# Optimization experiments

Measured on AMD Instinct MI355X. Metric: run time of the kernel, lower is better.

## Reference

```python
import jax, jax.numpy as jnp
import numpy as np

S = 8192        # total packed tokens
HID = 3072      # hidden_size
NHQ = 24        # query heads
NHKV = 8        # kv heads (GQA)
HD = 128        # head dim
NM = 2          # modalities (experts); tokens assumed modality-sorted: first half mod0, second half mod1
CHUNK = 1024    # ranged attention: 8 equal q/k ranges (block-diagonal)
NB = S // CHUNK
EPS = 1e-6


def setup_inputs() -> dict:
    key = jax.random.key(0)
    ks = jax.random.split(key, 4)
    s = 0.02
    qkv_out = (NHQ + 2 * NHKV) * HD
    # rotary tables: cos/sin of shape (S, HD/2)
    pos = jnp.arange(S, dtype=jnp.float32)
    inv_freq = 1.0 / (10000.0 ** (jnp.arange(0, HD, 2, dtype=jnp.float32) / HD))
    freqs = pos[:, None] * inv_freq[None, :]
    return {
        "x": jax.random.normal(ks[0], (S, HID), jnp.float32),
        "w_qkv": jax.random.normal(ks[1], (NM, qkv_out, HID), jnp.float32) * s,
        "b_qkv": jnp.zeros((NM, qkv_out), jnp.float32),
        "q_norm_w": jnp.zeros((NM, HD), jnp.float32),
        "k_norm_w": jnp.zeros((NM, HD), jnp.float32),
        "cos": jnp.cos(freqs),
        "sin": jnp.sin(freqs),
        "w_out": jax.random.normal(ks[2], (NM, HID, NHQ * HD), jnp.float32) * s,
        "b_out": jnp.zeros((NM, HID), jnp.float32),
    }


def _rms(t):
    # MultiModalityRMSNorm.rms: fp32 rsqrt(mean(x^2)+eps)
    return t * jax.lax.rsqrt(jnp.mean(t * t, axis=-1, keepdims=True) + EPS)


def _rotate_half(t):
    x1, x2 = jnp.split(t, 2, axis=-1)
    return jnp.concatenate([-x2, x1], axis=-1)


def reference(x, w_qkv, b_qkv, q_norm_w, k_norm_w, cos, sin, w_out, b_out):
    half = S // NM
    xm = x.reshape(NM, half, HID)                        # modality-dispatched tokens
    # per-modality (MoE) qkv projection: [m, t, out]
    qkv = jnp.einsum('mti,moi->mto', xm, w_qkv) + b_qkv[:, None, :]
    q, k, v = jnp.split(qkv, [NHQ * HD, (NHQ + NHKV) * HD], axis=-1)
    q = q.reshape(NM, half, NHQ, HD)
    k = k.reshape(NM, half, NHKV, HD)
    v = v.reshape(NM, half, NHKV, HD)
    # per-modality QK RMSNorm over head_dim, weight init zeros -> scale (w+1)
    q = _rms(q) * (q_norm_w[:, None, None, :] + 1.0)
    k = _rms(k) * (k_norm_w[:, None, None, :] + 1.0)
    # RoPE (non-interleaved): cos/sin (S, HD/2) -> (m, t, 1, HD) via (2 d) repeat
    cosm = cos.reshape(NM, half, HD // 2)
    sinm = sin.reshape(NM, half, HD // 2)
    cos2 = jnp.concatenate([cosm, cosm], axis=-1)[:, :, None, :]
    sin2 = jnp.concatenate([sinm, sinm], axis=-1)[:, :, None, :]
    q = q * cos2 + _rotate_half(q) * sin2
    k = k * cos2 + _rotate_half(k) * sin2
    # undispatch back to packed token order (modality-sorted identity permutation)
    qs = q.reshape(S, NHQ, HD)
    ks = k.reshape(S, NHKV, HD)
    vs = v.reshape(S, NHKV, HD)
    # ranged (block-diagonal) flash attention: NB equal q/k ranges of CHUNK tokens
    qb = qs.reshape(NB, CHUNK, NHQ, HD)
    kb = jnp.repeat(ks.reshape(NB, CHUNK, NHKV, HD), NHQ // NHKV, axis=2)  # GQA expand
    vb = jnp.repeat(vs.reshape(NB, CHUNK, NHKV, HD), NHQ // NHKV, axis=2)
    scale = HD ** -0.5
    scores = jnp.einsum('bqhd,bkhd->bhqk', qb, kb) * scale
    attn = jax.nn.softmax(scores, axis=-1)
    ob = jnp.einsum('bhqk,bkhd->bqhd', attn, vb)
    o = ob.reshape(NM, half, NHQ * HD)
    # per-modality output projection
    out = jnp.einsum('mti,moi->mto', o, w_out) + b_out[:, None, :]
    return out.reshape(S, HID)
```

## Files before the change

kernel.cpp:

```cpp
#include <hip/hip_runtime.h>
#include <hip/hip_bf16.h>


typedef __bf16 bf16;
typedef __attribute__((ext_vector_type(8))) __bf16 bf16x8;
typedef __attribute__((ext_vector_type(4))) __bf16 bf16x4;
typedef __attribute__((ext_vector_type(4))) float f32x4;

#define S_TOT 8192
#define HID 3072
#define NHQ 24
#define NHKV 8
#define HD 128
#define QKV_OUT 5120
#define CHUNKT 1024

__device__ inline void gload_lds16(const void* g, void* l) {
  __builtin_amdgcn_global_load_lds((const __attribute__((address_space(1))) void*)g,
                                   (__attribute__((address_space(3))) void*)l, 16, 0, 0);
}

__device__ inline f32x4 mfma16(bf16x8 a, bf16x8 b, f32x4 c) {
  return __builtin_amdgcn_mfma_f32_16x16x32_bf16(a, b, c, 0, 0, 0);
}

__global__ __launch_bounds__(256) void cvt_kernel(const float* __restrict__ in,
                                                  bf16* __restrict__ out, int n4) {
  int idx = blockIdx.x * 256 + threadIdx.x;
  int stride = gridDim.x * 256;
  for (int i = idx; i < n4; i += stride) {
    float4 v = reinterpret_cast<const float4*>(in)[i];
    bf16x4 o = {(bf16)v.x, (bf16)v.y, (bf16)v.z, (bf16)v.w};
    reinterpret_cast<bf16x4*>(out)[i] = o;
  }
}

template <int OUT_BF16>
__global__ __launch_bounds__(512, 2) void gemm256(const bf16* __restrict__ A,
                                                  const bf16* __restrict__ B,
                                                  const float* __restrict__ bias,
                                                  void* __restrict__ Cv,
                                                  int M, int N, int K) {
  __shared__ bf16 lds[65536];
  const int tid = threadIdx.x;
  const int l = tid & 63;
  const int w = tid >> 6;
  const int wr = w >> 2, wc = w & 3;
  const int lm = l & 15, lg = l >> 4;

  const int nwg = gridDim.x;
  const int id = blockIdx.x;
  const int swzid = (id & 7) * (nwg >> 3) + (id >> 3);
  const int xt = N >> 8, yt = M >> 8;
  const int bn = swzid % xt;
  const int rem = swzid / xt;
  const int bm = rem % yt;
  const int mz = rem / yt;

  const bf16* Ag = A + (size_t)mz * M * K + (size_t)(bm * 256) * K;
  const bf16* Bg = B + (size_t)mz * N * K + (size_t)(bn * 256) * K;
  const float* biasg = bias + (size_t)mz * N;

  const int srow = tid >> 3;
  const int scolb = ((tid & 7) * 16) ^ ((srow & 7) << 4);
  const bf16* Asrc = Ag + (size_t)srow * K + (scolb >> 1);
  const bf16* Bsrc = Bg + (size_t)srow * K + (scolb >> 1);
  bf16* ldsA = lds;
  bf16* ldsB = lds + 32768;

  auto stA = [&](int buf, int q, int t) {
    gload_lds16(Asrc + (size_t)(q * 64) * K + t * 64,
                ldsA + buf * 16384 + q * 4096 + tid * 8);
  };
  auto stB = [&](int buf, int q, int t) {
    gload_lds16(Bsrc + (size_t)(q * 64) * K + t * 64,
                ldsB + buf * 16384 + q * 4096 + tid * 8);
  };

  const int xmb = (lm & 7) << 4;
  const int cb0 = (lg * 16) ^ xmb;
  const int cb1 = cb0 ^ 64;
  const int aoff0 = (wr * 128 + lm) * 64 + (cb0 >> 1);
  const int aoff1 = (wr * 128 + lm) * 64 + (cb1 >> 1);
  const int boff0 = (wc * 64 + lm) * 64 + (cb0 >> 1);
  const int boff1 = (wc * 64 + lm) * 64 + (cb1 >> 1);

  const int NT = K >> 6;
  f32x4 acc[8][4] = {};

#pragma unroll
  for (int q = 0; q < 4; ++q) stA(0, q, 0);
#pragma unroll
  for (int q = 0; q < 4; ++q) stB(0, q, 0);
#pragma unroll
  for (int q = 0; q < 4; ++q) stA(1, q, 1);
  stB(1, 0, 1);
  stB(1, 1, 1);
  asm volatile("s_waitcnt vmcnt(6)" ::: "memory");
  __builtin_amdgcn_s_barrier();

  for (int T = 0; T < NT; ++T) {
    const int cbuf = T & 1, nbuf = cbuf ^ 1;
    const bf16* Ac = ldsA + cbuf * 16384;
    const bf16* Bc = ldsB + cbuf * 16384;
    const bool s1 = (T + 1) < NT;
    const bool s2 = (T + 2) < NT;
    bf16x8 alo[4][2], ahi[4][2], blo[2][2], bhi[2][2];

#pragma unroll
    for (int i = 0; i < 4; ++i) {
      alo[i][0] = *(const bf16x8*)(Ac + aoff0 + i * 1024);
      alo[i][1] = *(const bf16x8*)(Ac + aoff1 + i * 1024);
    }
#pragma unroll
    for (int j = 0; j < 2; ++j) {
      blo[j][0] = *(const bf16x8*)(Bc + boff0 + j * 1024);
      blo[j][1] = *(const bf16x8*)(Bc + boff1 + j * 1024);
    }
    if (s1) { stB(nbuf, 2, T + 1); stB(nbuf, 3, T + 1); }
    __builtin_amdgcn_s_barrier();
    asm volatile("s_waitcnt lgkmcnt(0)" ::: "memory");
    __builtin_amdgcn_s_setprio(1);
#pragma unroll
    for (int i = 0; i < 4; ++i)
#pragma unroll
      for (int j = 0; j < 2; ++j) {
        acc[i][j] = mfma16(alo[i][0], blo[j][0], acc[i][j]);
        acc[i][j] = mfma16(alo[i][1], blo[j][1], acc[i][j]);
      }
    __builtin_amdgcn_s_setprio(0);
    __builtin_amdgcn_s_barrier();

#pragma unroll
    for (int j = 0; j < 2; ++j) {
      bhi[j][0] = *(const bf16x8*)(Bc + boff0 + (j + 2) * 1024);
      bhi[j][1] = *(const bf16x8*)(Bc + boff1 + (j + 2) * 1024);
    }
    if (s2) { stA(cbuf, 0, T + 2); stA(cbuf, 2, T + 2); }
    __builtin_amdgcn_s_barrier();
    asm volatile("s_waitcnt lgkmcnt(0)" ::: "memory");
    __builtin_amdgcn_s_setprio(1);
#pragma unroll
    for (int i = 0; i < 4; ++i)
#pragma unroll
      for (int j = 0; j < 2; ++j) {
        acc[i][j + 2] = mfma16(alo[i][0], bhi[j][0], acc[i][j + 2]);
        acc[i][j + 2] = mfma16(alo[i][1], bhi[j][1], acc[i][j + 2]);
      }
    __builtin_amdgcn_s_setprio(0);
    __builtin_amdgcn_s_barrier();

#pragma unroll
    for (int i = 0; i < 4; ++i) {
      ahi[i][0] = *(const bf16x8*)(Ac + aoff0 + (i + 4) * 1024);
      ahi[i][1] = *(const bf16x8*)(Ac + aoff1 + (i + 4) * 1024);
    }
    if (s2) { stB(cbuf, 0, T + 2); stB(cbuf, 1, T + 2); }
    __builtin_amdgcn_s_barrier();
    asm volatile("s_waitcnt lgkmcnt(0)" ::: "memory");
    __builtin_amdgcn_s_setprio(1);
#pragma unroll
    for (int i = 0; i < 4; ++i)
#pragma unroll
      for (int j = 0; j < 2; ++j) {
        acc[i + 4][j] = mfma16(ahi[i][0], blo[j][0], acc[i + 4][j]);
        acc[i + 4][j] = mfma16(ahi[i][1], blo[j][1], acc[i + 4][j]);
      }
    __builtin_amdgcn_s_setprio(0);
    __builtin_amdgcn_s_barrier();

    if (s2) { stA(cbuf, 1, T + 2); stA(cbuf, 3, T + 2); }
    __builtin_amdgcn_s_barrier();
    __builtin_amdgcn_s_setprio(1);
#pragma unroll
    for (int i = 0; i < 4; ++i)
#pragma unroll
      for (int j = 0; j < 2; ++j) {
        acc[i + 4][j + 2] = mfma16(ahi[i][0], bhi[j][0], acc[i + 4][j + 2]);
        acc[i + 4][j + 2] = mfma16(ahi[i][1], bhi[j][1], acc[i + 4][j + 2]);
      }
    __builtin_amdgcn_s_setprio(0);
    if (s2)
      asm volatile("s_waitcnt vmcnt(6)" ::: "memory");
    else
      asm volatile("s_waitcnt vmcnt(0)" ::: "memory");
    __builtin_amdgcn_s_barrier();
  }

  const int row0 = bm * 256 + wr * 128 + lg * 4;
  const int col0 = bn * 256 + wc * 64 + lm;
#pragma unroll
  for (int j = 0; j < 4; ++j) {
    const int col = col0 + j * 16;
    const float bv = biasg[col];
#pragma unroll
    for (int i = 0; i < 8; ++i)
#pragma unroll
      for (int r = 0; r < 4; ++r) {
        const int row = row0 + i * 16 + r;
        const float v = acc[i][j][r] + bv;
        if (OUT_BF16)
          ((bf16*)Cv)[(size_t)mz * M * N + (size_t)row * N + col] = (bf16)v;
        else
          ((float*)Cv)[(size_t)mz * M * N + (size_t)row * N + col] = v;
      }
  }
}

__global__ __launch_bounds__(256) void rmsrope_kernel(bf16* __restrict__ qkv,
                                                      const float* __restrict__ qw,
                                                      const float* __restrict__ kw,
                                                      const float* __restrict__ cosT,
                                                      const float* __restrict__ sinT) {
  int gid = blockIdx.x * 4 + (threadIdx.x >> 6);
  int l = threadIdx.x & 63;
  int tok = gid >> 5;
  int slot = gid & 31;
  int mz = tok >> 12;
  bf16* p;
  const float* wv;
  if (slot < NHQ) {
    p = qkv + (size_t)tok * QKV_OUT + slot * HD;
    wv = qw + mz * HD;
  } else {
    p = qkv + (size_t)tok * QKV_OUT + HID + (slot - NHQ) * HD;
    wv = kw + mz * HD;
  }
  int d = l * 2;
  float x0 = (float)p[d];
  float x1 = (float)p[d + 1];
  float ss = x0 * x0 + x1 * x1;
#pragma unroll
  for (int m = 1; m < 64; m <<= 1) ss += __shfl_xor(ss, m);
  float rn = rsqrtf(ss * (1.0f / 128.0f) + 1e-6f);
  float n0 = x0 * rn * (wv[d] + 1.0f);
  float n1 = x1 * rn * (wv[d + 1] + 1.0f);
  float o0 = __shfl_xor(n0, 32);
  float o1 = __shfl_xor(n1, 32);
  int ci = d & 63;
  float2 cv = *reinterpret_cast<const float2*>(cosT + (size_t)tok * 64 + ci);
  float2 sv = *reinterpret_cast<const float2*>(sinT + (size_t)tok * 64 + ci);
  float sgn = (l < 32) ? -1.0f : 1.0f;
  p[d] = (bf16)(n0 * cv.x + sgn * o0 * sv.x);
  p[d + 1] = (bf16)(n1 * cv.y + sgn * o1 * sv.y);
}

__global__ __launch_bounds__(256) void attn_kernel(const bf16* __restrict__ qkv,
                                                   bf16* __restrict__ o) {
  constexpr float CEXP = 0.12753139626334912f;
  const int tid = threadIdx.x;
  const int l = tid & 63;
  const int w = tid >> 6;
  const int sq = blockIdx.x;
  const int h = blockIdx.y;
  const int blk = blockIdx.z;
  const int kvh = h / 3;
  const int qtok0 = blk * CHUNKT + sq * 128 + w * 32;
  const int ktok0 = blk * CHUNKT;

  __shared__ bf16 KP[128 * 136];
  __shared__ bf16 Vt[128 * 136];

  bf16x8 qf[2][4];
#pragma unroll
  for (int i = 0; i < 2; ++i) {
    const bf16* qp =
        qkv + (size_t)(qtok0 + i * 16 + (l & 15)) * QKV_OUT + h * HD + (l >> 4) * 8;
#pragma unroll
    for (int c = 0; c < 4; ++c) qf[i][c] = *reinterpret_cast<const bf16x8*>(qp + c * 32);
  }

  f32x4 of[2][8] = {};
  float mrow[2][4], lrow[2][4];
#pragma unroll
  for (int i = 0; i < 2; ++i)
#pragma unroll
    for (int r = 0; r < 4; ++r) {
      mrow[i][r] = -1e30f;
      lrow[i][r] = 0.0f;
    }

  for (int c = 0; c < 8; ++c) {
    __syncthreads();
    const int kt = ktok0 + c * 128;
#pragma unroll
    for (int it = 0; it < 8; ++it) {
      int task = it * 256 + tid;
      int key = task >> 4, dc = task & 15;
      *reinterpret_cast<bf16x8*>(&KP[key * 136 + dc * 8]) =
          *reinterpret_cast<const bf16x8*>(
              qkv + (size_t)(kt + key) * QKV_OUT + HID + kvh * HD + dc * 8);
    }
#pragma unroll
    for (int it = 0; it < 8; ++it) {
      int task = it * 256 + tid;
      int key = task & 127, dc = task >> 7;
      bf16x8 vv = *reinterpret_cast<const bf16x8*>(
          qkv + (size_t)(kt + key) * QKV_OUT + HID + NHKV * HD + kvh * HD + dc * 8);
#pragma unroll
      for (int jj = 0; jj < 8; ++jj) Vt[(dc * 8 + jj) * 136 + key] = vv[jj];
    }
    __syncthreads();

    f32x4 sacc[2][8] = {};
#pragma unroll
    for (int kd = 0; kd < 4; ++kd) {
      bf16x8 kb[8];
#pragma unroll
      for (int j = 0; j < 8; ++j)
        kb[j] = *reinterpret_cast<const bf16x8*>(
            &KP[(j * 16 + (l & 15)) * 136 + kd * 32 + (l >> 4) * 8]);
#pragma unroll
      for (int i = 0; i < 2; ++i)
#pragma unroll
        for (int j = 0; j < 8; ++j) sacc[i][j] = mfma16(qf[i][kd], kb[j], sacc[i][j]);
    }

    float alpha[2][4];
#pragma unroll
    for (int i = 0; i < 2; ++i) {
#pragma unroll
      for (int r = 0; r < 4; ++r) {
        float mx = sacc[i][0][r];
#pragma unroll
        for (int j = 1; j < 8; ++j) mx = fmaxf(mx, sacc[i][j][r]);
        mx = fmaxf(mx, __shfl_xor(mx, 1));
        mx = fmaxf(mx, __shfl_xor(mx, 2));
        mx = fmaxf(mx, __shfl_xor(mx, 4));
        mx = fmaxf(mx, __shfl_xor(mx, 8));
        float mnew = fmaxf(mrow[i][r], mx);
        float al = exp2f((mrow[i][r] - mnew) * CEXP);
        mrow[i][r] = mnew;
        float ps = 0.0f;
#pragma unroll
        for (int j = 0; j < 8; ++j) {
          float pv = exp2f((sacc[i][j][r] - mnew) * CEXP);
          sacc[i][j][r] = pv;
          ps += pv;
        }
        ps += __shfl_xor(ps, 1);
        ps += __shfl_xor(ps, 2);
        ps += __shfl_xor(ps, 4);
        ps += __shfl_xor(ps, 8);
        lrow[i][r] = lrow[i][r] * al + ps;
        alpha[i][r] = al;
      }
    }
#pragma unroll
    for (int i = 0; i < 2; ++i)
#pragma unroll
      for (int j = 0; j < 8; ++j)
#pragma unroll
        for (int r = 0; r < 4; ++r) of[i][j][r] *= alpha[i][r];

    __syncthreads();
    bf16* P = KP + w * (32 * 136);
#pragma unroll
    for (int i = 0; i < 2; ++i)
#pragma unroll
      for (int j = 0; j < 8; ++j)
#pragma unroll
        for (int r = 0; r < 4; ++r)
          P[(i * 16 + (l >> 4) * 4 + r) * 136 + j * 16 + (l & 15)] = (bf16)sacc[i][j][r];

#pragma unroll
    for (int kk = 0; kk < 4; ++kk) {
      bf16x8 pa[2];
#pragma unroll
      for (int i = 0; i < 2; ++i)
        pa[i] = *reinterpret_cast<const bf16x8*>(
            &P[(i * 16 + (l & 15)) * 136 + kk * 32 + (l >> 4) * 8]);
#pragma unroll
      for (int j = 0; j < 8; ++j) {
        bf16x8 bv = *reinterpret_cast<const bf16x8*>(
            &Vt[(j * 16 + (l & 15)) * 136 + kk * 32 + (l >> 4) * 8]);
        of[0][j] = mfma16(pa[0], bv, of[0][j]);
        of[1][j] = mfma16(pa[1], bv, of[1][j]);
      }
    }
  }

#pragma unroll
  for (int i = 0; i < 2; ++i) {
#pragma unroll
    for (int r = 0; r < 4; ++r) {
      float inv = 1.0f / lrow[i][r];
      int row = qtok0 + i * 16 + (l >> 4) * 4 + r;
      bf16* orow = o + (size_t)row * HID + h * HD + (l & 15);
#pragma unroll
      for (int j = 0; j < 8; ++j) orow[j * 16] = (bf16)(of[i][j][r] * inv);
    }
  }
}

extern "C" void kernel_launch(void* const* d_in, const int* in_sizes, int n_in,
                              void* d_out, int out_size, void* d_ws, size_t ws_size,
                              hipStream_t stream) {
  const float* x = (const float*)d_in[0];
  const float* wqkv = (const float*)d_in[1];
  const float* bqkv = (const float*)d_in[2];
  const float* qnw = (const float*)d_in[3];
  const float* knw = (const float*)d_in[4];
  const float* cosT = (const float*)d_in[5];
  const float* sinT = (const float*)d_in[6];
  const float* wout = (const float*)d_in[7];
  const float* bout = (const float*)d_in[8];
  float* out = (float*)d_out;

  char* ws = (char*)d_ws;
  bf16* xb = (bf16*)ws;
  ws += (size_t)S_TOT * HID * 2;
  bf16* wqkvb = (bf16*)ws;
  ws += (size_t)2 * QKV_OUT * HID * 2;
  bf16* qkv = (bf16*)ws;
  bf16* ob = xb;
  bf16* woutb = wqkvb;

  cvt_kernel<<<2048, 256, 0, stream>>>(x, xb, S_TOT * HID / 4);
  cvt_kernel<<<2048, 256, 0, stream>>>(wqkv, wqkvb, 2 * QKV_OUT * HID / 4);

  gemm256<1><<<(QKV_OUT / 256) * (4096 / 256) * 2, 512, 0, stream>>>(
      xb, wqkvb, bqkv, qkv, 4096, QKV_OUT, HID);

  cvt_kernel<<<2048, 256, 0, stream>>>(wout, woutb, 2 * HID * HID / 4);

  rmsrope_kernel<<<(S_TOT * (NHQ + NHKV)) / 4, 256, 0, stream>>>(qkv, qnw, knw, cosT, sinT);

  attn_kernel<<<dim3(8, NHQ, 8), 256, 0, stream>>>(qkv, ob);

  gemm256<0><<<(HID / 256) * (4096 / 256) * 2, 512, 0, stream>>>(
      ob, woutb, bout, out, 4096, HID, HID);
}
```

Measured before the change: 1.136 ms.

## Double-buffer K/V tiles with register prefetch and XOR-swizzled LDS in attention

The attention kernel now processes 64-key tiles instead of 128, keeps two LDS buffers for K and V, and prefetches the next tile into registers during compute. It writes that tile to the alternate buffer after the PV step, so there is one barrier per iteration instead of three. Padded LDS rows are replaced by XOR swizzles on K, transposed V and a dedicated per-wave P buffer, and s_setprio wraps the MFMA bursts. The goal is to hide global-load latency and cut LDS bank conflicts and syncs. The cost is more registers for the prefetch, which could reduce occupancy.

After: 1.237 ms. +9.0%, slower.

```diff
diff --git a/kernel.cpp b/kernel.cpp
--- a/kernel.cpp
+++ b/kernel.cpp
@@ -248,27 +248,64 @@
 __global__ __launch_bounds__(256) void attn_kernel(const bf16* __restrict__ qkv,
                                                    bf16* __restrict__ o) {
   constexpr float CEXP = 0.12753139626334912f;
+  constexpr int NCH = CHUNKT / 64;
   const int tid = threadIdx.x;
   const int l = tid & 63;
   const int w = tid >> 6;
+  const int lm = l & 15, lg = l >> 4;
   const int sq = blockIdx.x;
   const int h = blockIdx.y;
   const int blk = blockIdx.z;
   const int kvh = h / 3;
   const int qtok0 = blk * CHUNKT + sq * 128 + w * 32;
-  const int ktok0 = blk * CHUNKT;
-
-  __shared__ bf16 KP[128 * 136];
-  __shared__ bf16 Vt[128 * 136];
+
+  __shared__ bf16 Ks[2][64 * 128];
+  __shared__ bf16 Vs[2][128 * 64];
+  __shared__ bf16 Ps[4][32 * 64];
 
   bf16x8 qf[2][4];
 #pragma unroll
   for (int i = 0; i < 2; ++i) {
-    const bf16* qp =
-        qkv + (size_t)(qtok0 + i * 16 + (l & 15)) * QKV_OUT + h * HD + (l >> 4) * 8;
+    const bf16* qp = qkv + (size_t)(qtok0 + i * 16 + lm) * QKV_OUT + h * HD + lg * 8;
 #pragma unroll
     for (int c = 0; c < 4; ++c) qf[i][c] = *reinterpret_cast<const bf16x8*>(qp + c * 32);
   }
+
+  const bf16* Kg = qkv + (size_t)(blk * CHUNKT) * QKV_OUT + HID + kvh * HD;
+  const bf16* Vg = Kg + NHKV * HD;
+  const int krow = tid >> 4;
+  const int kdc8 = (tid & 15) * 8;
+  const int vkey = tid & 63;
+  const int vdc0 = tid >> 6;
+
+  bf16x8 kreg[4], vreg[4];
+  auto loadKV = [&](int c) {
+    const bf16* kp = Kg + (size_t)(c * 64) * QKV_OUT;
+    const bf16* vp = Vg + (size_t)(c * 64) * QKV_OUT;
+#pragma unroll
+    for (int it = 0; it < 4; ++it)
+      kreg[it] = *reinterpret_cast<const bf16x8*>(
+          kp + (size_t)(it * 16 + krow) * QKV_OUT + kdc8);
+#pragma unroll
+    for (int it = 0; it < 4; ++it)
+      vreg[it] = *reinterpret_cast<const bf16x8*>(
+          vp + (size_t)vkey * QKV_OUT + (it * 4 + vdc0) * 8);
+  };
+  auto writeKV = [&](int buf) {
+#pragma unroll
+    for (int it = 0; it < 4; ++it) {
+      int key = it * 16 + krow;
+      *reinterpret_cast<bf16x8*>(&Ks[buf][key * 128 + (kdc8 ^ ((key & 7) << 3))]) =
+          kreg[it];
+    }
+#pragma unroll
+    for (int it = 0; it < 4; ++it) {
+      int d0 = (it * 4 + vdc0) * 8;
+#pragma unroll
+      for (int jj = 0; jj < 8; ++jj)
+        Vs[buf][(d0 + jj) * 64 + (vkey ^ (jj << 3))] = vreg[it][jj];
+    }
+  };
 
   f32x4 of[2][8] = {};
   float mrow[2][4], lrow[2][4];
@@ -280,40 +317,32 @@
       lrow[i][r] = 0.0f;
     }
 
-  for (int c = 0; c < 8; ++c) {
-    __syncthreads();
-    const int kt = ktok0 + c * 128;
-#pragma unroll
-    for (int it = 0; it < 8; ++it) {
-      int task = it * 256 + tid;
-      int key = task >> 4, dc = task & 15;
-      *reinterpret_cast<bf16x8*>(&KP[key * 136 + dc * 8]) =
-          *reinterpret_cast<const bf16x8*>(
-              qkv + (size_t)(kt + key) * QKV_OUT + HID + kvh * HD + dc * 8);
-    }
-#pragma unroll
-    for (int it = 0; it < 8; ++it) {
-      int task = it * 256 + tid;
-      int key = task & 127, dc = task >> 7;
-      bf16x8 vv = *reinterpret_cast<const bf16x8*>(
-          qkv + (size_t)(kt + key) * QKV_OUT + HID + NHKV * HD + kvh * HD + dc * 8);
-#pragma unroll
-      for (int jj = 0; jj < 8; ++jj) Vt[(dc * 8 + jj) * 136 + key] = vv[jj];
-    }
-    __syncthreads();
-
-    f32x4 sacc[2][8] = {};
+  loadKV(0);
+  writeKV(0);
+  __syncthreads();
+
+  const int swz = (lm & 7) << 3;
+  for (int c = 0; c < NCH; ++c) {
+    const int cur = c & 1;
+    if (c + 1 < NCH) loadKV(c + 1);
+    const bf16* Kc = Ks[cur];
+    const bf16* Vc = Vs[cur];
+    bf16* Pw = Ps[w];
+
+    f32x4 sacc[2][4] = {};
 #pragma unroll
     for (int kd = 0; kd < 4; ++kd) {
-      bf16x8 kb[8];
-#pragma unroll
-      for (int j = 0; j < 8; ++j)
+      bf16x8 kb[4];
+#pragma unroll
+      for (int j = 0; j < 4; ++j)
         kb[j] = *reinterpret_cast<const bf16x8*>(
-            &KP[(j * 16 + (l & 15)) * 136 + kd * 32 + (l >> 4) * 8]);
+            Kc + (j * 16 + lm) * 128 + ((kd * 32 + lg * 8) ^ swz));
+      __builtin_amdgcn_s_setprio(1);
 #pragma unroll
       for (int i = 0; i < 2; ++i)
 #pragma unroll
-        for (int j = 0; j < 8; ++j) sacc[i][j] = mfma16(qf[i][kd], kb[j], sacc[i][j]);
+        for (int j = 0; j < 4; ++j) sacc[i][j] = mfma16(qf[i][kd], kb[j], sacc[i][j]);
+      __builtin_amdgcn_s_setprio(0);
     }
 
     float alpha[2][4];
@@ -323,7 +352,7 @@
       for (int r = 0; r < 4; ++r) {
         float mx = sacc[i][0][r];
 #pragma unroll
-        for (int j = 1; j < 8; ++j) mx = fmaxf(mx, sacc[i][j][r]);
+        for (int j = 1; j < 4; ++j) mx = fmaxf(mx, sacc[i][j][r]);
         mx = fmaxf(mx, __shfl_xor(mx, 1));
         mx = fmaxf(mx, __shfl_xor(mx, 2));
         mx = fmaxf(mx, __shfl_xor(mx, 4));
@@ -333,7 +362,7 @@
         mrow[i][r] = mnew;
         float ps = 0.0f;
 #pragma unroll
-        for (int j = 0; j < 8; ++j) {
+        for (int j = 0; j < 4; ++j) {
           float pv = exp2f((sacc[i][j][r] - mnew) * CEXP);
           sacc[i][j][r] = pv;
           ps += pv;
@@ -353,31 +382,36 @@
 #pragma unroll
         for (int r = 0; r < 4; ++r) of[i][j][r] *= alpha[i][r];
 
-    __syncthreads();
-    bf16* P = KP + w * (32 * 136);
 #pragma unroll
     for (int i = 0; i < 2; ++i)
 #pragma unroll
-      for (int j = 0; j < 8; ++j)
-#pragma unroll
-        for (int r = 0; r < 4; ++r)
-          P[(i * 16 + (l >> 4) * 4 + r) * 136 + j * 16 + (l & 15)] = (bf16)sacc[i][j][r];
-
-#pragma unroll
-    for (int kk = 0; kk < 4; ++kk) {
+      for (int j = 0; j < 4; ++j)
+#pragma unroll
+        for (int r = 0; r < 4; ++r) {
+          int q = i * 16 + lg * 4 + r;
+          Pw[q * 64 + ((j * 16 + lm) ^ ((q & 7) << 3))] = (bf16)sacc[i][j][r];
+        }
+
+#pragma unroll
+    for (int kk = 0; kk < 2; ++kk) {
       bf16x8 pa[2];
 #pragma unroll
       for (int i = 0; i < 2; ++i)
         pa[i] = *reinterpret_cast<const bf16x8*>(
-            &P[(i * 16 + (l & 15)) * 136 + kk * 32 + (l >> 4) * 8]);
+            Pw + (i * 16 + lm) * 64 + ((kk * 32 + lg * 8) ^ swz));
+      __builtin_amdgcn_s_setprio(1);
 #pragma unroll
       for (int j = 0; j < 8; ++j) {
         bf16x8 bv = *reinterpret_cast<const bf16x8*>(
-            &Vt[(j * 16 + (l & 15)) * 136 + kk * 32 + (l >> 4) * 8]);
+            Vc + (j * 16 + lm) * 64 + ((kk * 32 + lg * 8) ^ swz));
         of[0][j] = mfma16(pa[0], bv, of[0][j]);
         of[1][j] = mfma16(pa[1], bv, of[1][j]);
       }
-    }
+      __builtin_amdgcn_s_setprio(0);
+    }
+
+    if (c + 1 < NCH) writeKV(cur ^ 1);
+    __syncthreads();
   }
 
 #pragma unroll
@@ -385,8 +419,8 @@
 #pragma unroll
     for (int r = 0; r < 4; ++r) {
       float inv = 1.0f / lrow[i][r];
-      int row = qtok0 + i * 16 + (l >> 4) * 4 + r;
-      bf16* orow = o + (size_t)row * HID + h * HD + (l & 15);
+      int row = qtok0 + i * 16 + lg * 4 + r;
+      bf16* orow = o + (size_t)row * HID + h * HD + lm;
 #pragma unroll
       for (int j = 0; j < 8; ++j) orow[j * 16] = (bf16)(of[i][j][r] * inv);
     }
```
